# Kernel optimization log

Hardware: AMD Instinct MI355X
Metric: run time of the kernel (lower is better)

The kernel has to match this reference:

```python
import jax, jax.numpy as jnp
import numpy as np
import math

HIDDEN = 2048
HIGHWAY_BIAS = 0.0
# rescale=True, has_skip_term=True, num_matrices=3 -> residual scaled by sqrt(1+2*exp(bias))
SCALE_X = (1.0 + 2.0 * math.exp(HIGHWAY_BIAS)) ** 0.5


def setup_inputs() -> dict:
    key = jax.random.key(0)
    k1, k2, k3 = jax.random.split(key, 3)
    L, B, D = 1024, 8, HIDDEN
    x = jax.random.normal(k1, (L, B, D), dtype=jnp.float32)
    c0 = jnp.zeros((B, D), dtype=jnp.float32)
    # Xavier-like init scale as in reset_parameters (uniform +-sqrt(3/D))
    val_range = (3.0 / D) ** 0.5
    weight = jax.random.uniform(k2, (D, 3 * D), dtype=jnp.float32,
                                minval=-val_range, maxval=val_range)
    weight_c = jax.random.uniform(k3, (2 * D,), dtype=jnp.float32,
                                  minval=-(3.0 ** 0.5), maxval=3.0 ** 0.5) * (0.5 ** 0.5)
    bias = jnp.concatenate([jnp.zeros((D,), jnp.float32),
                            jnp.full((D,), HIGHWAY_BIAS, jnp.float32)])
    return {"x": x, "c0": c0, "weight": weight, "weight_c": weight_c, "bias": bias}


def _sru_forward(x, c0, weight, weight_c, bias):
    L, B, D = x.shape
    # U = x @ W  -> [L, B, 3, D]; num_matrices=3 (input_size == output_size)
    U = jnp.einsum('lbi,ij->lbj', x, weight).reshape(L, B, D, 3)
    u0 = U[..., 0]  # candidate
    u1 = U[..., 1]  # forget gate pre-activation
    u2 = U[..., 2]  # reset/highway gate pre-activation
    vf, vr = weight_c[:D], weight_c[D:]
    bf, br = bias[:D], bias[D:]

    def step(c_prev, inp):
        u0t, u1t, u2t, xt = inp
        f = jax.nn.sigmoid(u1t + vf * c_prev + bf)
        c_t = (c_prev - u0t) * f + u0t
        r = jax.nn.sigmoid(u2t + vr * c_t + br)
        # activation 'none': g(c_t) = c_t; skip term = x * scale_x
        h_t = r * c_t + (1.0 - r) * xt * SCALE_X
        return c_t, h_t

    c_last, h = jax.lax.scan(step, c0, (u0, u1, u2, x))
    return h, c_last


def reference(x, c0, weight, weight_c, bias):
    return _sru_forward(x, c0, weight, weight_c, bias)
```

## Files before the change

### kernel.cpp

```cpp
#include <hip/hip_runtime.h>
#include <stdint.h>

#define L_SEQ 1024
#define BATCH 8
#define DIM   2048
#define GM    8192
#define GN    6144
#define GK    2048
#define SCALE_X 1.7320508075688772f
#define SCAN_PF 16

using bf16x8  = __attribute__((ext_vector_type(8))) __bf16;
using floatx4 = __attribute__((ext_vector_type(4))) float;

__device__ __forceinline__ unsigned short f2bf(float f) {
  unsigned u = __float_as_uint(f);
  u += 0x7FFFu + ((u >> 16) & 1u);
  return (unsigned short)(u >> 16);
}
__device__ __forceinline__ float sigmoidf_fast(float z) {
  return __builtin_amdgcn_rcpf(1.0f + __expf(-z));
}
__device__ __forceinline__ void async16(const unsigned short* g, unsigned short* l) {
  __builtin_amdgcn_global_load_lds(
      (__attribute__((address_space(1))) unsigned int*)g,
      (__attribute__((address_space(3))) unsigned int*)l,
      16, 0, 0);
}

__global__ __launch_bounds__(256) void cast_x_kernel(const float4* __restrict__ xin,
                                                     unsigned short* __restrict__ Aout) {
  const int n4 = (GM * GK) / 4;
  for (int i = blockIdx.x * blockDim.x + threadIdx.x; i < n4; i += gridDim.x * blockDim.x) {
    float4 v = xin[i];
    union { unsigned short s[4]; unsigned long long ll; } o;
    o.s[0] = f2bf(v.x); o.s[1] = f2bf(v.y); o.s[2] = f2bf(v.z); o.s[3] = f2bf(v.w);
    *(unsigned long long*)&Aout[(size_t)i * 4] = o.ll;
  }
}

__global__ __launch_bounds__(256) void transpose_w_kernel(const float* __restrict__ W,
                                                          unsigned short* __restrict__ Bt) {
  __shared__ float tile[32][33];
  const int tx = threadIdx.x & 31, ty = threadIdx.x >> 5;
  const int n0 = blockIdx.x * 32;
  const int k0 = blockIdx.y * 32;
#pragma unroll
  for (int r = 0; r < 32; r += 8)
    tile[ty + r][tx] = W[(size_t)(k0 + ty + r) * GN + n0 + tx];
  __syncthreads();
#pragma unroll
  for (int r = 0; r < 32; r += 8) {
    const int n = n0 + ty + r;
    const int dq = n / 3, j = n - 3 * dq;
    const int np = (j == 0) ? dq : (DIM + 2 * dq + (j - 1));
    Bt[(size_t)np * GK + k0 + tx] = f2bf(tile[tx][ty + r]);
  }
}

__global__ __launch_bounds__(256) void gemm_kernel(const unsigned short* __restrict__ A,
                                                   const unsigned short* __restrict__ Bt,
                                                   unsigned short* __restrict__ U) {
  __shared__ alignas(16) unsigned short As[128 * 32];
  __shared__ alignas(16) unsigned short Bs[128 * 32];
  const int tid  = threadIdx.x;
  const int wave = tid >> 6, lane = tid & 63;
  const int quad = lane >> 4, lrow = lane & 15;
  const int wm = (wave >> 1) * 64, wn = (wave & 1) * 64;
  const int mBase = blockIdx.y * 128, nBase = blockIdx.x * 128;

  floatx4 acc[4][4] = {};

  const int o0 = tid * 16;
  const int r0 = o0 >> 6;
  const int c0e = (o0 & 63) >> 1;
  const unsigned short* aG0 = A  + (size_t)(mBase + r0)      * GK + c0e;
  const unsigned short* aG1 = A  + (size_t)(mBase + r0 + 64) * GK + c0e;
  const unsigned short* bG0 = Bt + (size_t)(nBase + r0)      * GK + c0e;
  const unsigned short* bG1 = Bt + (size_t)(nBase + r0 + 64) * GK + c0e;
  unsigned short* asL0 = &As[o0 >> 1];
  unsigned short* asL1 = &As[(o0 >> 1) + 2048];
  unsigned short* bsL0 = &Bs[o0 >> 1];
  unsigned short* bsL1 = &Bs[(o0 >> 1) + 2048];

  for (int k0 = 0; k0 < GK; k0 += 32) {
    async16(aG0 + k0, asL0);
    async16(aG1 + k0, asL1);
    async16(bG0 + k0, bsL0);
    async16(bG1 + k0, bsL1);
    __syncthreads();

    bf16x8 aF[4], bF[4];
#pragma unroll
    for (int t = 0; t < 4; ++t) {
      aF[t] = *(const bf16x8*)&As[(wm + t * 16 + lrow) * 32 + quad * 8];
      bF[t] = *(const bf16x8*)&Bs[(wn + t * 16 + lrow) * 32 + quad * 8];
    }
#pragma unroll
    for (int mt = 0; mt < 4; ++mt)
#pragma unroll
      for (int nt = 0; nt < 4; ++nt)
        acc[mt][nt] = __builtin_amdgcn_mfma_f32_16x16x32_bf16(aF[mt], bF[nt], acc[mt][nt], 0, 0, 0);
    __syncthreads();
  }

#pragma unroll
  for (int mt = 0; mt < 4; ++mt) {
    const int gm = mBase + wm + mt * 16 + quad * 4;
#pragma unroll
    for (int nt = 0; nt < 4; ++nt) {
      const int gn = nBase + wn + nt * 16 + lrow;
#pragma unroll
      for (int r = 0; r < 4; ++r)
        U[(size_t)(gm + r) * GN + gn] = f2bf(acc[mt][nt][r]);
    }
  }
}

__global__ __launch_bounds__(64) void sru_scan_kernel(const unsigned short* __restrict__ U,
                                                      const unsigned short* __restrict__ xbf,
                                                      const float* __restrict__ c0,
                                                      const float* __restrict__ wc,
                                                      const float* __restrict__ bias,
                                                      float* __restrict__ out) {
  const int e = blockIdx.x * 64 + threadIdx.x;
  const int b = e >> 11, d = e & (DIM - 1);
  const float vf = wc[d], vr = wc[DIM + d];
  const float bfv = bias[d], brv = bias[DIM + d];
  float c = c0[e];

  constexpr int PF = SCAN_PF;
  constexpr int US = BATCH * GN;
  constexpr int XS = BATCH * DIM;

  const unsigned short* u0p  = U + (size_t)b * GN + d;
  const unsigned short* u12p = U + (size_t)b * GN + DIM + 2 * d;
  const unsigned short* xp   = xbf + (size_t)b * DIM + d;
  float* hp = out + (size_t)b * DIM + d;

  unsigned pu0[PF], pu12[PF], pux[PF];
#pragma unroll
  for (int j = 0; j < PF; ++j) {
    pu0[j]  = u0p[(size_t)j * US];
    pu12[j] = *(const unsigned*)(u12p + (size_t)j * US);
    pux[j]  = xp[(size_t)j * XS];
  }
  const unsigned short* uf0  = u0p + (size_t)PF * US;
  const unsigned short* uf12 = u12p + (size_t)PF * US;
  const unsigned short* xf   = xp + (size_t)PF * XS;

  for (int l0 = 0; l0 < L_SEQ; l0 += PF) {
#pragma unroll
    for (int j = 0; j < PF; ++j) {
      const unsigned r0 = pu0[j], r12 = pu12[j], rx = pux[j];
      pu0[j]  = uf0[0];
      pu12[j] = *(const unsigned*)uf12;
      pux[j]  = xf[0];
      uf0 += US; uf12 += US; xf += XS;
      const float a0 = __uint_as_float(r0 << 16);
      const float u1 = __uint_as_float(r12 << 16);
      const float u2 = __uint_as_float(r12 & 0xFFFF0000u);
      const float ax = __uint_as_float(rx << 16) * SCALE_X;
      const float f = sigmoidf_fast(u1 + fmaf(vf, c, bfv));
      c = fmaf(c - a0, f, a0);
      const float r = sigmoidf_fast(u2 + fmaf(vr, c, brv));
      *hp = fmaf(r, c - ax, ax);
      hp += XS;
    }
  }
  out[(size_t)L_SEQ * XS + e] = c;
}

extern "C" void kernel_launch(void* const* d_in, const int* in_sizes, int n_in,
                              void* d_out, int out_size, void* d_ws, size_t ws_size,
                              hipStream_t stream) {
  const float* x    = (const float*)d_in[0];
  const float* c0   = (const float*)d_in[1];
  const float* W    = (const float*)d_in[2];
  const float* wc   = (const float*)d_in[3];
  const float* bias = (const float*)d_in[4];
  float* out = (float*)d_out;

  char* ws = (char*)d_ws;
  unsigned short* A_bf  = (unsigned short*)(ws);
  unsigned short* Bt_bf = (unsigned short*)(ws + 34078720);
  unsigned short* U_bf  = (unsigned short*)(ws + 59244544);

  cast_x_kernel<<<4096, 256, 0, stream>>>((const float4*)x, A_bf);
  transpose_w_kernel<<<dim3(GN / 32, GK / 32), 256, 0, stream>>>(W, Bt_bf);
  gemm_kernel<<<dim3(GN / 128, GM / 128), 256, 0, stream>>>(A_bf, Bt_bf, U_bf);
  sru_scan_kernel<<<256, 64, 0, stream>>>(U_bf, A_bf, c0, wc, bias, out);
}
```

Measured before the change: 484.6 us.

## Interleave x into U layout for scan and deepen GEMM K-tile with LDS swizzle

The GEMM now loads 64-wide K tiles per sync with an XOR-swizzled LDS layout, which halves the number of barriers and reduces bank conflicts. The cast kernel also writes bf16 x interleaved next to the candidate column in a widened U buffer (row stride 8192). This lets the scan do two 32-bit loads per step instead of three scattered loads. The cost is a larger workspace, strided 2-byte scatter writes in the cast kernel, and a fallback path when the workspace is too small.

```diff
diff --git a/kernel.cpp b/kernel.cpp
--- a/kernel.cpp
+++ b/kernel.cpp
@@ -9,6 +9,7 @@
 #define GK    2048
 #define SCALE_X 1.7320508075688772f
 #define SCAN_PF 16
+#define W_ILV  8192
 
 using bf16x8  = __attribute__((ext_vector_type(8))) __bf16;
 using floatx4 = __attribute__((ext_vector_type(4))) float;
@@ -28,14 +29,22 @@
       16, 0, 0);
 }
 
+template <bool ILV>
 __global__ __launch_bounds__(256) void cast_x_kernel(const float4* __restrict__ xin,
-                                                     unsigned short* __restrict__ Aout) {
+                                                     unsigned short* __restrict__ Aout,
+                                                     unsigned short* __restrict__ Ux) {
   const int n4 = (GM * GK) / 4;
   for (int i = blockIdx.x * blockDim.x + threadIdx.x; i < n4; i += gridDim.x * blockDim.x) {
     float4 v = xin[i];
     union { unsigned short s[4]; unsigned long long ll; } o;
     o.s[0] = f2bf(v.x); o.s[1] = f2bf(v.y); o.s[2] = f2bf(v.z); o.s[3] = f2bf(v.w);
     *(unsigned long long*)&Aout[(size_t)i * 4] = o.ll;
+    if (ILV) {
+      const int f = i * 4;
+      const int gm = f >> 11, d = f & (DIM - 1);
+      unsigned short* dst = Ux + (size_t)gm * W_ILV + 2 * d + 1;
+      dst[0] = o.s[0]; dst[2] = o.s[1]; dst[4] = o.s[2]; dst[6] = o.s[3];
+    }
   }
 }
 
@@ -58,11 +67,12 @@
   }
 }
 
+template <bool ILV>
 __global__ __launch_bounds__(256) void gemm_kernel(const unsigned short* __restrict__ A,
                                                    const unsigned short* __restrict__ Bt,
                                                    unsigned short* __restrict__ U) {
-  __shared__ alignas(16) unsigned short As[128 * 32];
-  __shared__ alignas(16) unsigned short Bs[128 * 32];
+  __shared__ alignas(16) unsigned short As[128 * 64];
+  __shared__ alignas(16) unsigned short Bs[128 * 64];
   const int tid  = threadIdx.x;
   const int wave = tid >> 6, lane = tid & 63;
   const int quad = lane >> 4, lrow = lane & 15;
@@ -71,58 +81,109 @@
 
   floatx4 acc[4][4] = {};
 
-  const int o0 = tid * 16;
-  const int r0 = o0 >> 6;
-  const int c0e = (o0 & 63) >> 1;
-  const unsigned short* aG0 = A  + (size_t)(mBase + r0)      * GK + c0e;
-  const unsigned short* aG1 = A  + (size_t)(mBase + r0 + 64) * GK + c0e;
-  const unsigned short* bG0 = Bt + (size_t)(nBase + r0)      * GK + c0e;
-  const unsigned short* bG1 = Bt + (size_t)(nBase + r0 + 64) * GK + c0e;
-  unsigned short* asL0 = &As[o0 >> 1];
-  unsigned short* asL1 = &As[(o0 >> 1) + 2048];
-  unsigned short* bsL0 = &Bs[o0 >> 1];
-  unsigned short* bsL1 = &Bs[(o0 >> 1) + 2048];
-
-  for (int k0 = 0; k0 < GK; k0 += 32) {
-    async16(aG0 + k0, asL0);
-    async16(aG1 + k0, asL1);
-    async16(bG0 + k0, bsL0);
-    async16(bG1 + k0, bsL1);
+  const int r  = tid >> 3;
+  const int sC = tid & 7;
+  const int cg = sC ^ (r & 7);
+  const unsigned short* aG0 = A  + (size_t)(mBase + r) * GK + cg * 8;
+  const unsigned short* bG0 = Bt + (size_t)(nBase + r) * GK + cg * 8;
+  unsigned short* asD = &As[tid * 8];
+  unsigned short* bsD = &Bs[tid * 8];
+  const int swz = lrow & 7;
+
+  for (int k0 = 0; k0 < GK; k0 += 64) {
+#pragma unroll
+    for (int i = 0; i < 4; ++i) async16(aG0 + (size_t)i * 32 * GK + k0, asD + i * 2048);
+#pragma unroll
+    for (int i = 0; i < 4; ++i) async16(bG0 + (size_t)i * 32 * GK + k0, bsD + i * 2048);
     __syncthreads();
 
-    bf16x8 aF[4], bF[4];
-#pragma unroll
-    for (int t = 0; t < 4; ++t) {
-      aF[t] = *(const bf16x8*)&As[(wm + t * 16 + lrow) * 32 + quad * 8];
-      bF[t] = *(const bf16x8*)&Bs[(wn + t * 16 + lrow) * 32 + quad * 8];
-    }
-#pragma unroll
-    for (int mt = 0; mt < 4; ++mt)
-#pragma unroll
-      for (int nt = 0; nt < 4; ++nt)
-        acc[mt][nt] = __builtin_amdgcn_mfma_f32_16x16x32_bf16(aF[mt], bF[nt], acc[mt][nt], 0, 0, 0);
+#pragma unroll
+    for (int kk = 0; kk < 2; ++kk) {
+      const int s = (kk * 4 + quad) ^ swz;
+      bf16x8 aF[4], bF[4];
+#pragma unroll
+      for (int t = 0; t < 4; ++t) {
+        aF[t] = *(const bf16x8*)&As[(wm + t * 16 + lrow) * 64 + s * 8];
+        bF[t] = *(const bf16x8*)&Bs[(wn + t * 16 + lrow) * 64 + s * 8];
+      }
+#pragma unroll
+      for (int mt = 0; mt < 4; ++mt)
+#pragma unroll
+        for (int nt = 0; nt < 4; ++nt)
+          acc[mt][nt] = __builtin_amdgcn_mfma_f32_16x16x32_bf16(aF[mt], bF[nt], acc[mt][nt], 0, 0, 0);
+    }
     __syncthreads();
   }
 
+  const int rowW = ILV ? W_ILV : GN;
 #pragma unroll
   for (int mt = 0; mt < 4; ++mt) {
     const int gm = mBase + wm + mt * 16 + quad * 4;
 #pragma unroll
     for (int nt = 0; nt < 4; ++nt) {
       const int gn = nBase + wn + nt * 16 + lrow;
-#pragma unroll
-      for (int r = 0; r < 4; ++r)
-        U[(size_t)(gm + r) * GN + gn] = f2bf(acc[mt][nt][r]);
-    }
-  }
-}
-
-__global__ __launch_bounds__(64) void sru_scan_kernel(const unsigned short* __restrict__ U,
-                                                      const unsigned short* __restrict__ xbf,
-                                                      const float* __restrict__ c0,
-                                                      const float* __restrict__ wc,
-                                                      const float* __restrict__ bias,
-                                                      float* __restrict__ out) {
+      const int col = ILV ? ((gn < DIM) ? 2 * gn : gn + DIM) : gn;
+#pragma unroll
+      for (int q = 0; q < 4; ++q)
+        U[(size_t)(gm + q) * rowW + col] = f2bf(acc[mt][nt][q]);
+    }
+  }
+}
+
+__global__ __launch_bounds__(64) void sru_scan_ilv(const unsigned short* __restrict__ U,
+                                                   const float* __restrict__ c0,
+                                                   const float* __restrict__ wc,
+                                                   const float* __restrict__ bias,
+                                                   float* __restrict__ out) {
+  const int e = blockIdx.x * 64 + threadIdx.x;
+  const int b = e >> 11, d = e & (DIM - 1);
+  const float vf = wc[d], vr = wc[DIM + d];
+  const float bfv = bias[d], brv = bias[DIM + d];
+  float c = c0[e];
+
+  constexpr int PF = SCAN_PF;
+  constexpr int UD = BATCH * W_ILV / 2;
+  constexpr int XS = BATCH * DIM;
+
+  const unsigned* u0x = (const unsigned*)(U + (size_t)b * W_ILV + 2 * d);
+  const unsigned* u12 = (const unsigned*)(U + (size_t)b * W_ILV + 2 * DIM + 2 * d);
+  float* hp = out + (size_t)b * DIM + d;
+
+  unsigned p0x[PF], p12[PF];
+#pragma unroll
+  for (int j = 0; j < PF; ++j) {
+    p0x[j] = u0x[(size_t)j * UD];
+    p12[j] = u12[(size_t)j * UD];
+  }
+  const unsigned* f0x = u0x + (size_t)PF * UD;
+  const unsigned* f12 = u12 + (size_t)PF * UD;
+
+  for (int l0 = 0; l0 < L_SEQ; l0 += PF) {
+#pragma unroll
+    for (int j = 0; j < PF; ++j) {
+      const unsigned ra = p0x[j], rb = p12[j];
+      p0x[j] = *f0x; p12[j] = *f12;
+      f0x += UD; f12 += UD;
+      const float a0 = __uint_as_float(ra << 16);
+      const float ax = __uint_as_float(ra & 0xFFFF0000u) * SCALE_X;
+      const float u1 = __uint_as_float(rb << 16);
+      const float u2 = __uint_as_float(rb & 0xFFFF0000u);
+      const float f = sigmoidf_fast(u1 + fmaf(vf, c, bfv));
+      c = fmaf(c - a0, f, a0);
+      const float rr = sigmoidf_fast(u2 + fmaf(vr, c, brv));
+      *hp = fmaf(rr, c - ax, ax);
+      hp += XS;
+    }
+  }
+  out[(size_t)L_SEQ * XS + e] = c;
+}
+
+__global__ __launch_bounds__(64) void sru_scan_flat(const unsigned short* __restrict__ U,
+                                                    const unsigned short* __restrict__ xbf,
+                                                    const float* __restrict__ c0,
+                                                    const float* __restrict__ wc,
+                                                    const float* __restrict__ bias,
+                                                    float* __restrict__ out) {
   const int e = blockIdx.x * 64 + threadIdx.x;
   const int b = e >> 11, d = e & (DIM - 1);
   const float vf = wc[d], vr = wc[DIM + d];
@@ -163,8 +224,8 @@
       const float ax = __uint_as_float(rx << 16) * SCALE_X;
       const float f = sigmoidf_fast(u1 + fmaf(vf, c, bfv));
       c = fmaf(c - a0, f, a0);
-      const float r = sigmoidf_fast(u2 + fmaf(vr, c, brv));
-      *hp = fmaf(r, c - ax, ax);
+      const float rr = sigmoidf_fast(u2 + fmaf(vr, c, brv));
+      *hp = fmaf(rr, c - ax, ax);
       hp += XS;
     }
   }
@@ -182,12 +243,23 @@
   float* out = (float*)d_out;
 
   char* ws = (char*)d_ws;
-  unsigned short* A_bf  = (unsigned short*)(ws);
-  unsigned short* Bt_bf = (unsigned short*)(ws + 34078720);
-  unsigned short* U_bf  = (unsigned short*)(ws + 59244544);
-
-  cast_x_kernel<<<4096, 256, 0, stream>>>((const float4*)x, A_bf);
-  transpose_w_kernel<<<dim3(GN / 32, GK / 32), 256, 0, stream>>>(W, Bt_bf);
-  gemm_kernel<<<dim3(GN / 128, GM / 128), 256, 0, stream>>>(A_bf, Bt_bf, U_bf);
-  sru_scan_kernel<<<256, 64, 0, stream>>>(U_bf, A_bf, c0, wc, bias, out);
-}
+  const size_t ILV_NEED = 33554432u + 25165824u + 134217728u + 2097152u;
+
+  if (ws_size >= ILV_NEED) {
+    unsigned short* A_bf  = (unsigned short*)(ws);
+    unsigned short* Bt_bf = (unsigned short*)(ws + 33554432);
+    unsigned short* U_bf  = (unsigned short*)(ws + 58720256);
+    cast_x_kernel<true><<<4096, 256, 0, stream>>>((const float4*)x, A_bf, U_bf);
+    transpose_w_kernel<<<dim3(GN / 32, GK / 32), 256, 0, stream>>>(W, Bt_bf);
+    gemm_kernel<true><<<dim3(GN / 128, GM / 128), 256, 0, stream>>>(A_bf, Bt_bf, U_bf);
+    sru_scan_ilv<<<256, 64, 0, stream>>>(U_bf, c0, wc, bias, out);
+  } else {
+    unsigned short* A_bf  = (unsigned short*)(ws);
+    unsigned short* Bt_bf = (unsigned short*)(ws + 34078720);
+    unsigned short* U_bf  = (unsigned short*)(ws + 59244544);
+    cast_x_kernel<false><<<4096, 256, 0, stream>>>((const float4*)x, A_bf, nullptr);
+    transpose_w_kernel<<<dim3(GN / 32, GK / 32), 256, 0, stream>>>(W, Bt_bf);
+    gemm_kernel<false><<<dim3(GN / 128, GM / 128), 256, 0, stream>>>(A_bf, Bt_bf, U_bf);
+    sru_scan_flat<<<256, 64, 0, stream>>>(U_bf, A_bf, c0, wc, bias, out);
+  }
+}
```

Measured after the change: 478.0 us. Within noise of the previous version (-1.3%).
